# Performance work log

Hardware: AMD Instinct MI355X
Metric: run time of the kernel (lower is better)

The kernel has to match this reference:

```python
import jax, jax.numpy as jnp
import numpy as np

B, C, HD, NL, NP = 2, 256, 8, 4, 4
D = C // HD
SHAPES = np.array([[128, 128], [64, 64], [32, 32], [16, 16]], dtype=np.int64)
LV = int(SHAPES.prod(axis=1).sum())  # 21760
LQ = LV


def _bilinear(v_l, loc, Hl, Wl):
    # v_l: [B, HD, Nl, D]; loc: [B, Q, HD, P, 2] normalized to [0,1]
    # Matches torch grid_sample(bilinear, padding='zeros', align_corners=False)
    Bq, Q, _, P, _ = loc.shape
    x = loc[..., 0] * Wl - 0.5
    y = loc[..., 1] * Hl - 0.5
    x0f = jnp.floor(x)
    y0f = jnp.floor(y)
    lx, ly = x - x0f, y - y0f
    x0 = x0f.astype(jnp.int32)
    y0 = y0f.astype(jnp.int32)

    def corner(xi, yi, w):
        valid = (xi >= 0) & (xi < Wl) & (yi >= 0) & (yi < Hl)
        idx = jnp.clip(yi, 0, Hl - 1) * Wl + jnp.clip(xi, 0, Wl - 1)  # [B,Q,HD,P]
        idx = idx.transpose(0, 2, 1, 3).reshape(Bq, HD, Q * P)
        g = jnp.take_along_axis(v_l, idx[..., None], axis=2).reshape(Bq, HD, Q, P, D)
        wm = jnp.where(valid, w, 0.0).transpose(0, 2, 1, 3)[..., None]  # [B,HD,Q,P,1]
        return g * wm

    return (corner(x0, y0, (1 - lx) * (1 - ly))
            + corner(x0 + 1, y0, lx * (1 - ly))
            + corner(x0, y0 + 1, (1 - lx) * ly)
            + corner(x0 + 1, y0 + 1, lx * ly))


def _msda(query, reference_points, value, shapes, W_off, b_off, W_attn, b_attn, W_val, b_val, W_out, b_out):
    # value projection -> per-head layout [B, HD, Lv, D]
    v = (value @ W_val + b_val).reshape(B, LV, HD, D).transpose(0, 2, 1, 3)
    off = (query @ W_off + b_off).reshape(B, LQ, HD, NL, NP, 2)
    aw = jax.nn.softmax((query @ W_attn + b_attn).reshape(B, LQ, HD, NL * NP), axis=-1)
    aw = aw.reshape(B, LQ, HD, NL, NP)
    norm = jnp.asarray(shapes[:, ::-1].copy(), query.dtype)  # (W_l, H_l) per level
    # sampling locations: [B, Lq, HD, NL, NP, 2]
    loc = reference_points[:, :, None, :, None, :] + off / norm[None, None, None, :, None, :]
    out = jnp.zeros((B, HD, LQ, D), query.dtype)
    start = 0
    for l in range(NL):  # small static loop over feature levels
        Hl, Wl = int(shapes[l, 0]), int(shapes[l, 1])
        samp = _bilinear(v[:, :, start:start + Hl * Wl], loc[:, :, :, l], Hl, Wl)  # [B,HD,Q,P,D]
        out = out + jnp.einsum('bhqpd,bhqp->bhqd', samp, aw[:, :, :, l].transpose(0, 2, 1, 3))
        start += Hl * Wl
    out = out.transpose(0, 2, 1, 3).reshape(B, LQ, C)
    # output projection + residual (identity = query, dropout inactive at eval)
    return out @ W_out + b_out + query


def setup_inputs():
    key = jax.random.key(0)
    ks = jax.random.split(key, 8)
    sc = 1.0 / np.sqrt(C)
    return {
        "query": jax.random.normal(ks[0], (B, LQ, C), jnp.float32),
        "reference_points": jax.random.uniform(ks[1], (B, LQ, NL, 2), dtype=jnp.float32),
        "value": jax.random.normal(ks[2], (B, LV, C), jnp.float32),
        "spatial_shapes": SHAPES,
        "level_start_index": np.concatenate([[0], np.cumsum(SHAPES.prod(axis=1))[:-1]]).astype(np.int64),
        "W_off": jax.random.normal(ks[3], (C, HD * NL * NP * 2), jnp.float32) * 0.01,
        "b_off": jax.random.normal(ks[4], (HD * NL * NP * 2,), jnp.float32) * 0.01,
        "W_attn": jax.random.normal(ks[5], (C, HD * NL * NP), jnp.float32) * 0.02,
        "b_attn": jnp.zeros((HD * NL * NP,), jnp.float32),
        "W_val": jax.random.normal(ks[6], (C, C), jnp.float32) * sc,
        "b_val": jnp.zeros((C,), jnp.float32),
        "W_out": jax.random.normal(ks[7], (C, C), jnp.float32) * sc,
        "b_out": jnp.zeros((C,), jnp.float32),
    }


def reference(query, reference_points, value, spatial_shapes, level_start_index, W_off, b_off, W_attn, b_attn, W_val, b_val, W_out, b_out):
    shapes = np.asarray(spatial_shapes)  # static level geometry
    del level_start_index  # level offsets derived directly from shapes
    return _msda(query, reference_points, value, shapes, W_off, b_off, W_attn, b_attn, W_val, b_val, W_out, b_out)
```

## Files before the change

### kernel.cpp

```cpp
#include <hip/hip_runtime.h>

#define LQN 21760
#define LVN 21760
#define BATCH 2
#define CDIM 256
#define HDN 8
#define DDIM 32
#define PADCELLS 22736

typedef __attribute__((ext_vector_type(8))) short short8;
typedef __attribute__((ext_vector_type(4))) float f32x4;
typedef __attribute__((ext_vector_type(2))) float f32x2;

__device__ __forceinline__ unsigned short f2bf(float f) {
  union { float f; unsigned int u; } v; v.f = f;
  unsigned int r = v.u + 0x7fffu + ((v.u >> 16) & 1u);
  return (unsigned short)(r >> 16);
}
__device__ __forceinline__ float bflo(unsigned int u) {
  union { unsigned int u; float f; } v; v.u = u << 16; return v.f;
}
__device__ __forceinline__ float bfhi(unsigned int u) {
  union { unsigned int u; float f; } v; v.u = u & 0xffff0000u; return v.f;
}
__device__ __forceinline__ unsigned pk2bf(float lo, float hi) {
  unsigned r;
  asm("v_cvt_pk_bf16_f32 %0, %1, %2" : "=v"(r) : "v"(lo), "v"(hi));
  return r;
}

template <int IMM>
__device__ __forceinline__ float swzf(float v) {
  return __int_as_float(__builtin_amdgcn_ds_swizzle(__float_as_int(v), IMM));
}
template <int IMM>
__device__ __forceinline__ unsigned swzu(unsigned v) {
  return (unsigned)__builtin_amdgcn_ds_swizzle((int)v, IMM);
}

__global__ __launch_bounds__(256) void prep_zero_kernel(
    const float* __restrict__ Wval, const float* __restrict__ Woff,
    const float* __restrict__ Wattn, const float* __restrict__ Wout,
    unsigned short* __restrict__ wtval, unsigned short* __restrict__ wtoa,
    unsigned short* __restrict__ wtout, unsigned short* __restrict__ vbf) {
  const int b = blockIdx.x;
  if (b < 384) {
    const int idx = b * 256 + threadIdx.x;
    const int n = idx >> 8, k = idx & 255;
    if (idx < 65536) {
      wtval[idx] = f2bf(Wval[k * 256 + n]);
      wtout[idx] = f2bf(Wout[k * 256 + n]);
    }
    const float v = (n < 256) ? Woff[k * 256 + n] : Wattn[k * 128 + (n - 256)];
    wtoa[idx] = f2bf(v);
  } else {
    const int b2 = b - 384;
    const int img = b2 >> 4;
    const int tid = (b2 & 15) * 256 + threadIdx.x;
    const int cell = tid >> 2;
    const int chunk = tid & 3;
    if (cell >= 976) return;
    const int lvl = (cell >= 516) + (cell >= 776) + (cell >= 908);
    const int base = (lvl == 0) ? 0 : (lvl == 1) ? 516 : (lvl == 2) ? 776 : 908;
    const int W2 = (lvl == 0) ? 130 : (lvl == 1) ? 66 : (lvl == 2) ? 34 : 18;
    const int pst = (lvl == 0) ? 0 : (lvl == 1) ? 16900 : (lvl == 2) ? 21256 : 22412;
    const int bb = cell - base;
    int x, y;
    if (bb < W2) { y = 0; x = bb; }
    else if (bb < 2 * W2) { y = W2 - 1; x = bb - W2; }
    else { const int r = bb - 2 * W2; y = 1 + (r >> 1); x = (r & 1) ? (W2 - 1) : 0; }
    const size_t off = (((size_t)img * PADCELLS + pst + y * W2 + x) << 5) + chunk * 8;
    *(uint4*)(vbf + off) = (uint4){0u, 0u, 0u, 0u};
  }
}

template <int MODE>
__device__ __forceinline__ void gemm_body(
    unsigned short* lsA0, unsigned short* lsB0, const int bx, const int by,
    const float* __restrict__ Af32, const unsigned short* __restrict__ Abf,
    const unsigned short* __restrict__ Wt, const float* __restrict__ bias0,
    const float* __restrict__ bias1, const float* __restrict__ resid,
    unsigned short* __restrict__ out_bf, float* __restrict__ out_f32) {
  constexpr int K = 256;
  constexpr int LDSS = 40;
  constexpr int LBUF = 128 * LDSS;
  const int m0 = bx * 128;
  const int n0 = by * 128;
  const int t = threadIdx.x;
  const int w = t >> 6;
  const int l = t & 63;
  const int wr = (w >> 1) * 64;
  const int wc = (w & 1) * 64;
  const int fr = l & 15;
  const int kk = (l >> 4) * 8;

  f32x4 acc[4][4];
#pragma unroll
  for (int mi = 0; mi < 4; ++mi)
#pragma unroll
    for (int ci = 0; ci < 4; ++ci) acc[mi][ci] = (f32x4){0.f, 0.f, 0.f, 0.f};

  const int ar8 = t >> 3, ak8 = (t & 7) * 4;
  const int ar4 = t >> 2, ak4 = (t & 3) * 8;

  float4 fa[4];
  uint4 ua2[2];
  uint4 ub[2];

#define LOADA(kt)                                                            \
  do {                                                                       \
    const int k0_ = (kt) * 32;                                               \
    if (MODE == 2) {                                                         \
      ua2[0] = *(const uint4*)(Abf + (size_t)(m0 + ar4) * K + k0_ + ak4);    \
      ua2[1] = *(const uint4*)(Abf + (size_t)(m0 + 64 + ar4) * K + k0_ + ak4);\
    } else {                                                                 \
      fa[0] = *(const float4*)(Af32 + (size_t)(m0 + ar8) * K + k0_ + ak8);   \
      fa[1] = *(const float4*)(Af32 + (size_t)(m0 + 32 + ar8) * K + k0_ + ak8);\
      fa[2] = *(const float4*)(Af32 + (size_t)(m0 + 64 + ar8) * K + k0_ + ak8);\
      fa[3] = *(const float4*)(Af32 + (size_t)(m0 + 96 + ar8) * K + k0_ + ak8);\
    }                                                                        \
    ub[0] = *(const uint4*)(Wt + (size_t)(n0 + ar4) * K + k0_ + ak4);        \
    ub[1] = *(const uint4*)(Wt + (size_t)(n0 + 64 + ar4) * K + k0_ + ak4);   \
  } while (0)

#define STOREL(buf)                                                          \
  do {                                                                       \
    unsigned short* la = lsA0 + (buf)*LBUF;                                  \
    unsigned short* lb = lsB0 + (buf)*LBUF;                                  \
    if (MODE == 2) {                                                         \
      *(uint4*)(la + ar4 * LDSS + ak4) = ua2[0];                             \
      *(uint4*)(la + (64 + ar4) * LDSS + ak4) = ua2[1];                      \
    } else {                                                                 \
      uint2 q;                                                               \
      q.x = pk2bf(fa[0].x, fa[0].y); q.y = pk2bf(fa[0].z, fa[0].w);          \
      *(uint2*)(la + ar8 * LDSS + ak8) = q;                                  \
      q.x = pk2bf(fa[1].x, fa[1].y); q.y = pk2bf(fa[1].z, fa[1].w);          \
      *(uint2*)(la + (32 + ar8) * LDSS + ak8) = q;                           \
      q.x = pk2bf(fa[2].x, fa[2].y); q.y = pk2bf(fa[2].z, fa[2].w);          \
      *(uint2*)(la + (64 + ar8) * LDSS + ak8) = q;                           \
      q.x = pk2bf(fa[3].x, fa[3].y); q.y = pk2bf(fa[3].z, fa[3].w);          \
      *(uint2*)(la + (96 + ar8) * LDSS + ak8) = q;                           \
    }                                                                        \
    *(uint4*)(lb + ar4 * LDSS + ak4) = ub[0];                                \
    *(uint4*)(lb + (64 + ar4) * LDSS + ak4) = ub[1];                         \
  } while (0)

  LOADA(0);
  STOREL(0);
  __syncthreads();

#pragma unroll
  for (int kt = 0; kt < 8; ++kt) {
    if (kt < 7) LOADA(kt + 1);
    const unsigned short* la = lsA0 + (kt & 1) * LBUF;
    const unsigned short* lb = lsB0 + (kt & 1) * LBUF;
    short8 af[4], bfr[4];
#pragma unroll
    for (int mi = 0; mi < 4; ++mi)
      af[mi] = *(const short8*)(la + (wr + mi * 16 + fr) * LDSS + kk);
#pragma unroll
    for (int ci = 0; ci < 4; ++ci)
      bfr[ci] = *(const short8*)(lb + (wc + ci * 16 + fr) * LDSS + kk);
#pragma unroll
    for (int mi = 0; mi < 4; ++mi)
#pragma unroll
      for (int ci = 0; ci < 4; ++ci)
        acc[mi][ci] = __builtin_amdgcn_mfma_f32_16x16x32_bf16(
            af[mi], bfr[ci], acc[mi][ci], 0, 0, 0);
    if (kt < 7) STOREL((kt + 1) & 1);
    __syncthreads();
  }
#undef LOADA
#undef STOREL

  const int fq = l >> 4;
  if (MODE == 0) {
    int rbase[16];
#pragma unroll
    for (int mi = 0; mi < 4; ++mi) {
#pragma unroll
      for (int r = 0; r < 4; ++r) {
        const int row = m0 + wr + mi * 16 + fq * 4 + r;
        const int bb = (row >= LVN) ? 1 : 0;
        const int i = row - bb * LVN;
        const int lvl = (i >= 16384) + (i >= 20480) + (i >= 21504);
        const int stl = (lvl == 0) ? 0 : (lvl == 1) ? 16384 : (lvl == 2) ? 20480 : 21504;
        const int pst = (lvl == 0) ? 0 : (lvl == 1) ? 16900 : (lvl == 2) ? 21256 : 22412;
        const int lw = 7 - lvl;
        const int Wl = 128 >> lvl;
        const int loc = i - stl;
        const int y = loc >> lw;
        const int x = loc & (Wl - 1);
        const int pidx = pst + (y + 1) * (Wl + 2) + (x + 1);
        rbase[mi * 4 + r] = bb * (HDN * PADCELLS * DDIM) + pidx * DDIM;
      }
    }
#pragma unroll
    for (int ci = 0; ci < 4; ++ci) {
      const int col = n0 + wc + ci * 16 + fr;
      const float bias = bias0[col];
      const int cterm = (col >> 5) * (PADCELLS * DDIM) + (col & 31);
#pragma unroll
      for (int mi = 0; mi < 4; ++mi) {
#pragma unroll
        for (int r = 0; r < 4; r += 2) {
          const unsigned u =
              pk2bf(acc[mi][ci][r] + bias, acc[mi][ci][r + 1] + bias);
          out_bf[(size_t)(rbase[mi * 4 + r] + cterm)] = (unsigned short)u;
          out_bf[(size_t)(rbase[mi * 4 + r + 1] + cterm)] =
              (unsigned short)(u >> 16);
        }
      }
    }
  } else if (MODE == 1) {
#pragma unroll
    for (int ci = 0; ci < 4; ++ci) {
      const int col = n0 + wc + ci * 16 + fr;
      const float bias = (col < 256) ? bias0[col] : bias1[col - 256];
#pragma unroll
      for (int mi = 0; mi < 4; ++mi) {
        const int row0 = m0 + wr + mi * 16 + fq * 4;
#pragma unroll
        for (int r = 0; r < 4; r += 2) {
          const unsigned u =
              pk2bf(acc[mi][ci][r] + bias, acc[mi][ci][r + 1] + bias);
          out_bf[(size_t)(row0 + r) * 384 + col] = (unsigned short)u;
          out_bf[(size_t)(row0 + r + 1) * 384 + col] = (unsigned short)(u >> 16);
        }
      }
    }
  } else {
#pragma unroll
    for (int ci = 0; ci < 4; ++ci) {
      const int col = n0 + wc + ci * 16 + fr;
      const float bias = bias0[col];
#pragma unroll
      for (int mi = 0; mi < 4; ++mi) {
#pragma unroll
        for (int r = 0; r < 4; ++r) {
          const int row = m0 + wr + mi * 16 + fq * 4 + r;
          const size_t o = (size_t)row * 256 + col;
          out_f32[o] = acc[mi][ci][r] + bias + resid[o];
        }
      }
    }
  }
}

__global__ __launch_bounds__(256) void gemm01_kernel(
    const float* __restrict__ value, const float* __restrict__ query,
    const unsigned short* __restrict__ wtval,
    const unsigned short* __restrict__ wtoa, const float* __restrict__ b_val,
    const float* __restrict__ b_off, const float* __restrict__ b_attn,
    unsigned short* __restrict__ vbf, unsigned short* __restrict__ offattn) {
  const int bid = blockIdx.x;
  const int q = bid / 40;
  const int rem = bid % 40;
  const int g = rem >> 3;
  const int r = rem & 7;
  const int u = q * 8 + r;
  if (u >= 340) return;
  __shared__ unsigned short lsA[2 * 128 * 40];
  __shared__ unsigned short lsB[2 * 128 * 40];
  if (g < 2) {
    gemm_body<0>(lsA, lsB, u, g, value, nullptr, wtval, b_val, nullptr,
                 nullptr, vbf, nullptr);
  } else {
    gemm_body<1>(lsA, lsB, u, g - 2, query, nullptr, wtoa, b_off, b_attn,
                 nullptr, offattn, nullptr);
  }
}

__global__ __launch_bounds__(256) void gemm2_kernel(
    const unsigned short* __restrict__ msout,
    const unsigned short* __restrict__ wtout, const float* __restrict__ b_out,
    const float* __restrict__ query, float* __restrict__ out) {
  const int bid = blockIdx.x;
  const int q = bid / 16;
  const int rem = bid % 16;
  const int y = rem >> 3;
  const int r = rem & 7;
  const int u = q * 8 + r;
  if (u >= 340) return;
  __shared__ unsigned short lsA[2 * 128 * 40];
  __shared__ unsigned short lsB[2 * 128 * 40];
  gemm_body<2>(lsA, lsB, u, y, nullptr, msout, wtout, b_out, nullptr, query,
               nullptr, out);
}

__global__ __launch_bounds__(256) void sampler_kernel(
    const unsigned short* __restrict__ vbf,
    const unsigned short* __restrict__ offattn,
    const float* __restrict__ refpts,
    unsigned short* __restrict__ msout) {
  const int lid = blockIdx.x;
  const int pair = lid & 7;
  const int k = lid >> 3;
  const int img = pair * 2 + (k & 1);
  const int qchunk = k >> 1;
  const int h = img & 7;
  const int bb = img >> 3;

  const int t = threadIdx.x;
  const int lane = t & 63;
  const int qloc = qchunk * 64 + (t >> 6) * 16 + (lane >> 2);
  const int qi = bb * LQN + qloc;
  const int j = lane & 3;
  const int d0 = j * 8;

  const unsigned short* oa = offattn + (size_t)qi * 384;

  const int Wl = 128 >> j;
  const int W2 = Wl + 2;
  const int pst = (j == 0) ? 0 : (j == 1) ? 16900 : (j == 2) ? 21256 : 22412;
  const float fw = (float)Wl;

  const uint2 lr = *(const uint2*)(oa + 256 + h * 16 + j * 4);
  const float l0 = bflo(lr.x), l1 = bfhi(lr.x);
  const float l2 = bflo(lr.y), l3 = bfhi(lr.y);
  float mx = fmaxf(fmaxf(l0, l1), fmaxf(l2, l3));
  mx = fmaxf(mx, swzf<0x041F>(mx));
  mx = fmaxf(mx, swzf<0x081F>(mx));
  const float e0v = __expf(l0 - mx), e1v = __expf(l1 - mx);
  const float e2v = __expf(l2 - mx), e3v = __expf(l3 - mx);
  float s = (e0v + e1v) + (e2v + e3v);
  s += swzf<0x041F>(s);
  s += swzf<0x081F>(s);
  const float inv = 1.f / s;
  const float aw4[4] = {e0v * inv, e1v * inv, e2v * inv, e3v * inv};

  const float2 rf = *(const float2*)(refpts + (size_t)qi * 8 + j * 2);
  const uint4 ov = *(const uint4*)(oa + h * 32 + j * 8);
  const unsigned op_[4] = {ov.x, ov.y, ov.z, ov.w};

  unsigned eo[4][4];
  float wt[4][4];
#pragma unroll
  for (int pt = 0; pt < 4; ++pt) {
    const float ox = bflo(op_[pt]);
    const float oy = bfhi(op_[pt]);
    const float xs = fmaf(rf.x, fw, ox) - 0.5f;
    const float ys = fmaf(rf.y, fw, oy) - 0.5f;
    const float x0f = floorf(xs), y0f = floorf(ys);
    const float lx = xs - x0f, ly = ys - y0f;
    const int x0 = (int)x0f, y0 = (int)y0f;
    const float a = aw4[pt];
    const float wy1 = a * ly, wy0 = a - wy1;
    const float w01v = wy0 * lx, w00v = wy0 - w01v;
    const float w11v = wy1 * lx, w10v = wy1 - w11v;
    const int xb0 = min(max(x0 + 1, 0), Wl + 1);
    const int xb1 = min(max(x0 + 2, 0), Wl + 1);
    const int yb0 = min(max(y0 + 1, 0), Wl + 1);
    const int yb1 = min(max(y0 + 2, 0), Wl + 1);
    const unsigned r0 = (unsigned)(pst + yb0 * W2);
    const unsigned r1 = (unsigned)(pst + yb1 * W2);
    eo[pt][0] = (r0 + xb0) << 5;
    eo[pt][1] = (r0 + xb1) << 5;
    eo[pt][2] = (r1 + xb0) << 5;
    eo[pt][3] = (r1 + xb1) << 5;
    wt[pt][0] = w00v; wt[pt][1] = w01v; wt[pt][2] = w10v; wt[pt][3] = w11v;
  }

  const unsigned headbase =
      (unsigned)img * (PADCELLS * DDIM) + (unsigned)d0;

  f32x2 acc0 = (f32x2){0.f, 0.f}, acc1 = (f32x2){0.f, 0.f};
  f32x2 acc2 = (f32x2){0.f, 0.f}, acc3 = (f32x2){0.f, 0.f};

#define ACCUM(rv, wgt)                                 \
  {                                                    \
    f32x2 v_;                                          \
    v_.x = bflo(rv.x); v_.y = bfhi(rv.x);              \
    acc0 += v_ * (wgt);                                \
    v_.x = bflo(rv.y); v_.y = bfhi(rv.y);              \
    acc1 += v_ * (wgt);                                \
    v_.x = bflo(rv.z); v_.y = bfhi(rv.z);              \
    acc2 += v_ * (wgt);                                \
    v_.x = bflo(rv.w); v_.y = bfhi(rv.w);              \
    acc3 += v_ * (wgt);                                \
  }

#define POINT(LVL, PT)                                                  \
  {                                                                     \
    constexpr int IMM = (LVL << 5) | 0x1C;                              \
    const unsigned o00 = swzu<IMM>(eo[PT][0]);                          \
    const unsigned o01 = swzu<IMM>(eo[PT][1]);                          \
    const unsigned o10 = swzu<IMM>(eo[PT][2]);                          \
    const unsigned o11 = swzu<IMM>(eo[PT][3]);                          \
    const float w00 = swzf<IMM>(wt[PT][0]);                             \
    const float w01 = swzf<IMM>(wt[PT][1]);                             \
    const float w10 = swzf<IMM>(wt[PT][2]);                             \
    const float w11 = swzf<IMM>(wt[PT][3]);                             \
    const uint4 v00 = *(const uint4*)(vbf + headbase + o00);            \
    const uint4 v01 = *(const uint4*)(vbf + headbase + o01);            \
    const uint4 v10 = *(const uint4*)(vbf + headbase + o10);            \
    const uint4 v11 = *(const uint4*)(vbf + headbase + o11);            \
    ACCUM(v00, w00)                                                     \
    ACCUM(v01, w01)                                                     \
    ACCUM(v10, w10)                                                     \
    ACCUM(v11, w11)                                                     \
  }

  POINT(0, 0) POINT(0, 1) POINT(0, 2) POINT(0, 3)
  POINT(1, 0) POINT(1, 1) POINT(1, 2) POINT(1, 3)
  POINT(2, 0) POINT(2, 1) POINT(2, 2) POINT(2, 3)
  POINT(3, 0) POINT(3, 1) POINT(3, 2) POINT(3, 3)
#undef POINT
#undef ACCUM

  uint4 outv;
  outv.x = pk2bf(acc0.x, acc0.y);
  outv.y = pk2bf(acc1.x, acc1.y);
  outv.z = pk2bf(acc2.x, acc2.y);
  outv.w = pk2bf(acc3.x, acc3.y);
  *(uint4*)(msout + (size_t)qi * 256 + h * 32 + d0) = outv;
}

extern "C" void kernel_launch(void* const* d_in, const int* in_sizes, int n_in,
                              void* d_out, int out_size, void* d_ws,
                              size_t ws_size, hipStream_t stream) {
  const float* query = (const float*)d_in[0];
  const float* refpts = (const float*)d_in[1];
  const float* value = (const float*)d_in[2];
  const float* W_off = (const float*)d_in[5];
  const float* b_off = (const float*)d_in[6];
  const float* W_attn = (const float*)d_in[7];
  const float* b_attn = (const float*)d_in[8];
  const float* W_val = (const float*)d_in[9];
  const float* b_val = (const float*)d_in[10];
  const float* W_out = (const float*)d_in[11];
  const float* b_out = (const float*)d_in[12];
  float* out = (float*)d_out;

  char* ws = (char*)d_ws;
  unsigned short* wtval = (unsigned short*)(ws);
  unsigned short* wtoa = (unsigned short*)(ws + 131072);
  unsigned short* wtout = (unsigned short*)(ws + 327680);
  unsigned short* vbf = (unsigned short*)(ws + 458752);
  unsigned short* offattn = (unsigned short*)(ws + 23740416);
  unsigned short* msout = (unsigned short*)(ws + 57163776);

  prep_zero_kernel<<<640, 256, 0, stream>>>(W_val, W_off, W_attn, W_out, wtval,
                                            wtoa, wtout, vbf);
  gemm01_kernel<<<1720, 256, 0, stream>>>(value, query, wtval, wtoa, b_val,
                                          b_off, b_attn, vbf, offattn);
  sampler_kernel<<<5440, 256, 0, stream>>>(vbf, offattn, refpts, msout);
  gemm2_kernel<<<688, 256, 0, stream>>>(msout, wtout, b_out, query, out);
}
```

Measured before the change: 150.2 us.

## Pack sampler corner offsets and weights, enlarge sampler blocks, move border zeroing

The sampler now packs two 16-bit corner cell indices per register and packs the bilinear weights as bf16 pairs. This halves the cross-lane swizzles per sampling point and reduces register pressure. Sampler blocks grow from 256 to 512 threads, covering 128 queries each, with half as many blocks. The zeroing of the padded value border moves from the prep kernel into extra blocks of the first GEMM kernel. The bf16 weights lower bilinear weight precision, and the 16-bit indices rely on per-level cell offsets staying below 65536.

```diff
diff --git a/kernel.cpp b/kernel.cpp
--- a/kernel.cpp
+++ b/kernel.cpp
@@ -38,40 +38,19 @@
   return (unsigned)__builtin_amdgcn_ds_swizzle((int)v, IMM);
 }
 
-__global__ __launch_bounds__(256) void prep_zero_kernel(
+__global__ __launch_bounds__(256) void prep_kernel(
     const float* __restrict__ Wval, const float* __restrict__ Woff,
     const float* __restrict__ Wattn, const float* __restrict__ Wout,
     unsigned short* __restrict__ wtval, unsigned short* __restrict__ wtoa,
-    unsigned short* __restrict__ wtout, unsigned short* __restrict__ vbf) {
-  const int b = blockIdx.x;
-  if (b < 384) {
-    const int idx = b * 256 + threadIdx.x;
-    const int n = idx >> 8, k = idx & 255;
-    if (idx < 65536) {
-      wtval[idx] = f2bf(Wval[k * 256 + n]);
-      wtout[idx] = f2bf(Wout[k * 256 + n]);
-    }
-    const float v = (n < 256) ? Woff[k * 256 + n] : Wattn[k * 128 + (n - 256)];
-    wtoa[idx] = f2bf(v);
-  } else {
-    const int b2 = b - 384;
-    const int img = b2 >> 4;
-    const int tid = (b2 & 15) * 256 + threadIdx.x;
-    const int cell = tid >> 2;
-    const int chunk = tid & 3;
-    if (cell >= 976) return;
-    const int lvl = (cell >= 516) + (cell >= 776) + (cell >= 908);
-    const int base = (lvl == 0) ? 0 : (lvl == 1) ? 516 : (lvl == 2) ? 776 : 908;
-    const int W2 = (lvl == 0) ? 130 : (lvl == 1) ? 66 : (lvl == 2) ? 34 : 18;
-    const int pst = (lvl == 0) ? 0 : (lvl == 1) ? 16900 : (lvl == 2) ? 21256 : 22412;
-    const int bb = cell - base;
-    int x, y;
-    if (bb < W2) { y = 0; x = bb; }
-    else if (bb < 2 * W2) { y = W2 - 1; x = bb - W2; }
-    else { const int r = bb - 2 * W2; y = 1 + (r >> 1); x = (r & 1) ? (W2 - 1) : 0; }
-    const size_t off = (((size_t)img * PADCELLS + pst + y * W2 + x) << 5) + chunk * 8;
-    *(uint4*)(vbf + off) = (uint4){0u, 0u, 0u, 0u};
-  }
+    unsigned short* __restrict__ wtout) {
+  const int idx = blockIdx.x * 256 + threadIdx.x;
+  const int n = idx >> 8, k = idx & 255;
+  if (idx < 65536) {
+    wtval[idx] = f2bf(Wval[k * 256 + n]);
+    wtout[idx] = f2bf(Wout[k * 256 + n]);
+  }
+  const float v = (n < 256) ? Woff[k * 256 + n] : Wattn[k * 128 + (n - 256)];
+  wtoa[idx] = f2bf(v);
 }
 
 template <int MODE>
@@ -254,6 +233,26 @@
     const float* __restrict__ b_off, const float* __restrict__ b_attn,
     unsigned short* __restrict__ vbf, unsigned short* __restrict__ offattn) {
   const int bid = blockIdx.x;
+  if (bid >= 1720) {
+    const int b2 = bid - 1720;
+    const int img = b2 >> 4;
+    const int tid = (b2 & 15) * 256 + threadIdx.x;
+    const int cell = tid >> 2;
+    const int chunk = tid & 3;
+    if (cell >= 976) return;
+    const int lvl = (cell >= 516) + (cell >= 776) + (cell >= 908);
+    const int base = (lvl == 0) ? 0 : (lvl == 1) ? 516 : (lvl == 2) ? 776 : 908;
+    const int W2 = (lvl == 0) ? 130 : (lvl == 1) ? 66 : (lvl == 2) ? 34 : 18;
+    const int pst = (lvl == 0) ? 0 : (lvl == 1) ? 16900 : (lvl == 2) ? 21256 : 22412;
+    const int bb = cell - base;
+    int x, y;
+    if (bb < W2) { y = 0; x = bb; }
+    else if (bb < 2 * W2) { y = W2 - 1; x = bb - W2; }
+    else { const int r = bb - 2 * W2; y = 1 + (r >> 1); x = (r & 1) ? (W2 - 1) : 0; }
+    const size_t off = (((size_t)img * PADCELLS + pst + y * W2 + x) << 5) + chunk * 8;
+    *(uint4*)(vbf + off) = (uint4){0u, 0u, 0u, 0u};
+    return;
+  }
   const int q = bid / 40;
   const int rem = bid % 40;
   const int g = rem >> 3;
@@ -288,7 +287,7 @@
                nullptr, out);
 }
 
-__global__ __launch_bounds__(256) void sampler_kernel(
+__global__ __launch_bounds__(512) void sampler_kernel(
     const unsigned short* __restrict__ vbf,
     const unsigned short* __restrict__ offattn,
     const float* __restrict__ refpts,
@@ -303,7 +302,7 @@
 
   const int t = threadIdx.x;
   const int lane = t & 63;
-  const int qloc = qchunk * 64 + (t >> 6) * 16 + (lane >> 2);
+  const int qloc = qchunk * 128 + (t >> 6) * 16 + (lane >> 2);
   const int qi = bb * LQN + qloc;
   const int j = lane & 3;
   const int d0 = j * 8;
@@ -333,8 +332,7 @@
   const uint4 ov = *(const uint4*)(oa + h * 32 + j * 8);
   const unsigned op_[4] = {ov.x, ov.y, ov.z, ov.w};
 
-  unsigned eo[4][4];
-  float wt[4][4];
+  unsigned cpkA[4], cpkB[4], wpkA[4], wpkB[4];
 #pragma unroll
   for (int pt = 0; pt < 4; ++pt) {
     const float ox = bflo(op_[pt]);
@@ -354,11 +352,10 @@
     const int yb1 = min(max(y0 + 2, 0), Wl + 1);
     const unsigned r0 = (unsigned)(pst + yb0 * W2);
     const unsigned r1 = (unsigned)(pst + yb1 * W2);
-    eo[pt][0] = (r0 + xb0) << 5;
-    eo[pt][1] = (r0 + xb1) << 5;
-    eo[pt][2] = (r1 + xb0) << 5;
-    eo[pt][3] = (r1 + xb1) << 5;
-    wt[pt][0] = w00v; wt[pt][1] = w01v; wt[pt][2] = w10v; wt[pt][3] = w11v;
+    cpkA[pt] = (r0 + xb0) | ((r0 + xb1) << 16);
+    cpkB[pt] = (r1 + xb0) | ((r1 + xb1) << 16);
+    wpkA[pt] = pk2bf(w00v, w01v);
+    wpkB[pt] = pk2bf(w10v, w11v);
   }
 
   const unsigned headbase =
@@ -383,18 +380,16 @@
 #define POINT(LVL, PT)                                                  \
   {                                                                     \
     constexpr int IMM = (LVL << 5) | 0x1C;                              \
-    const unsigned o00 = swzu<IMM>(eo[PT][0]);                          \
-    const unsigned o01 = swzu<IMM>(eo[PT][1]);                          \
-    const unsigned o10 = swzu<IMM>(eo[PT][2]);                          \
-    const unsigned o11 = swzu<IMM>(eo[PT][3]);                          \
-    const float w00 = swzf<IMM>(wt[PT][0]);                             \
-    const float w01 = swzf<IMM>(wt[PT][1]);                             \
-    const float w10 = swzf<IMM>(wt[PT][2]);                             \
-    const float w11 = swzf<IMM>(wt[PT][3]);                             \
-    const uint4 v00 = *(const uint4*)(vbf + headbase + o00);            \
-    const uint4 v01 = *(const uint4*)(vbf + headbase + o01);            \
-    const uint4 v10 = *(const uint4*)(vbf + headbase + o10);            \
-    const uint4 v11 = *(const uint4*)(vbf + headbase + o11);            \
+    const unsigned pA = swzu<IMM>(cpkA[PT]);                            \
+    const unsigned pB = swzu<IMM>(cpkB[PT]);                            \
+    const unsigned wA = swzu<IMM>(wpkA[PT]);                            \
+    const unsigned wB = swzu<IMM>(wpkB[PT]);                            \
+    const float w00 = bflo(wA), w01 = bfhi(wA);                         \
+    const float w10 = bflo(wB), w11 = bfhi(wB);                         \
+    const uint4 v00 = *(const uint4*)(vbf + headbase + ((pA & 0xFFFFu) << 5)); \
+    const uint4 v01 = *(const uint4*)(vbf + headbase + ((pA >> 16) << 5));     \
+    const uint4 v10 = *(const uint4*)(vbf + headbase + ((pB & 0xFFFFu) << 5)); \
+    const uint4 v11 = *(const uint4*)(vbf + headbase + ((pB >> 16) << 5));     \
     ACCUM(v00, w00)                                                     \
     ACCUM(v01, w01)                                                     \
     ACCUM(v10, w10)                                                     \
@@ -440,10 +435,10 @@
   unsigned short* offattn = (unsigned short*)(ws + 23740416);
   unsigned short* msout = (unsigned short*)(ws + 57163776);
 
-  prep_zero_kernel<<<640, 256, 0, stream>>>(W_val, W_off, W_attn, W_out, wtval,
-                                            wtoa, wtout, vbf);
-  gemm01_kernel<<<1720, 256, 0, stream>>>(value, query, wtval, wtoa, b_val,
+  prep_kernel<<<384, 256, 0, stream>>>(W_val, W_off, W_attn, W_out, wtval,
+                                       wtoa, wtout);
+  gemm01_kernel<<<1976, 256, 0, stream>>>(value, query, wtval, wtoa, b_val,
                                           b_off, b_attn, vbf, offattn);
-  sampler_kernel<<<5440, 256, 0, stream>>>(vbf, offattn, refpts, msout);
+  sampler_kernel<<<2720, 512, 0, stream>>>(vbf, offattn, refpts, msout);
   gemm2_kernel<<<688, 256, 0, stream>>>(msout, wtout, b_out, query, out);
 }
```

New measurement: 153.6 us. 2.3% more time.
